# Optimization experiments

Hardware: AMD Instinct MI355X
Metric: run time of the kernel (lower is better)

The kernel has to match this reference:

```python
import jax, jax.numpy as jnp
import numpy as np
from jax import lax

# mamba-130m-hf config
N_LAYERS = 24
D_MODEL = 768
D_INNER = 1536   # expand=2
D_STATE = 16
DT_RANK = 48     # ceil(768/16)
D_CONV = 4
VOCAB = 50280
ENC_DIM = 256
EPS = 1e-5
SEQ, BATCH = 512, 2  # input is (SEQ, BATCH, ENC_DIM); permute -> mamba batch=BATCH, seq=SEQ


def setup_inputs() -> dict:
    key = jax.random.key(0)
    ks = jax.random.split(key, 12)
    f = jnp.float32
    def rn(k, shape, scale=0.02):
        return (jax.random.normal(k, shape) * scale).astype(f)
    x = jax.random.normal(ks[0], (SEQ, BATCH, ENC_DIM), dtype=f)
    W_et = rn(ks[1], (D_MODEL, ENC_DIM))
    b_et = jnp.zeros((D_MODEL,), f)
    in_proj_w = rn(ks[2], (N_LAYERS, 2 * D_INNER, D_MODEL))
    conv_w = rn(ks[3], (N_LAYERS, D_INNER, D_CONV), 0.1)
    conv_b = jnp.zeros((N_LAYERS, D_INNER), f)
    x_proj_w = rn(ks[4], (N_LAYERS, DT_RANK + 2 * D_STATE, D_INNER))
    dt_proj_w = rn(ks[5], (N_LAYERS, D_INNER, DT_RANK), 0.1)
    # bias init so softplus(bias) lands in [1e-3, 1e-1] (standard mamba dt init)
    dt_init = jnp.exp(jax.random.uniform(ks[6], (N_LAYERS, D_INNER), minval=jnp.log(1e-3), maxval=jnp.log(1e-1)))
    dt_proj_b = jnp.log(jnp.expm1(dt_init)).astype(f)
    A_log = jnp.log(jnp.broadcast_to(jnp.arange(1, D_STATE + 1, dtype=f), (N_LAYERS, D_INNER, D_STATE))) * jnp.ones((1,), f)
    D = jnp.ones((N_LAYERS, D_INNER), f)
    out_proj_w = rn(ks[7], (N_LAYERS, D_MODEL, D_INNER))
    norm_w = jnp.ones((N_LAYERS, D_MODEL), f)
    final_norm_w = jnp.ones((D_MODEL,), f)
    embed = rn(ks[8], (VOCAB, D_MODEL))
    return {"x": x, "W_et": W_et, "b_et": b_et, "in_proj_w": in_proj_w, "conv_w": conv_w,
            "conv_b": conv_b, "x_proj_w": x_proj_w, "dt_proj_w": dt_proj_w, "dt_proj_b": dt_proj_b,
            "A_log": A_log, "D": D, "out_proj_w": out_proj_w, "norm_w": norm_w,
            "final_norm_w": final_norm_w, "embed": embed}


def rmsnorm(x, w):
    return x * lax.rsqrt(jnp.mean(x * x, axis=-1, keepdims=True) + EPS) * w


def mamba_layer(h, p):
    in_w, cw, cb, xw, dtw, dtb, Al, Dv, ow, nw = p
    hn = rmsnorm(h, nw)
    xz = hn @ in_w.T                       # (B,T,2*D_INNER)
    xi, z = jnp.split(xz, 2, axis=-1)
    # depthwise causal conv over time
    xc = lax.conv_general_dilated(xi.transpose(0, 2, 1), cw[:, None, :], (1,),
                                  [(D_CONV - 1, 0)], dimension_numbers=("NCH", "OIH", "NCH"),
                                  feature_group_count=D_INNER)
    xc = jax.nn.silu(xc + cb[None, :, None]).transpose(0, 2, 1)   # (B,T,D_INNER)
    proj = xc @ xw.T                                              # (B,T,DT_RANK+2*D_STATE)
    dt = jax.nn.softplus(proj[..., :DT_RANK] @ dtw.T + dtb)       # (B,T,D_INNER)
    Bm = proj[..., DT_RANK:DT_RANK + D_STATE]                     # (B,T,S)
    Cm = proj[..., DT_RANK + D_STATE:]                            # (B,T,S)
    A = -jnp.exp(Al)                                              # (D_INNER,S)
    dA = jnp.exp(dt[..., None] * A)                               # (B,T,D,S)
    dBx = dt[..., None] * Bm[:, :, None, :] * xc[..., None]       # (B,T,D,S)

    def step(hst, inp):
        a, bx, c = inp
        hst = a * hst + bx
        return hst, jnp.einsum("bds,bs->bd", hst, c)

    h0 = jnp.zeros(dA.shape[:1] + dA.shape[2:], dA.dtype)
    _, ys = lax.scan(step, h0, (dA.transpose(1, 0, 2, 3), dBx.transpose(1, 0, 2, 3), Cm.transpose(1, 0, 2)))
    y = ys.transpose(1, 0, 2) + Dv * xc
    y = y * jax.nn.silu(z)
    return h + y @ ow.T


def reference(x, W_et, b_et, in_proj_w, conv_w, conv_b, x_proj_w, dt_proj_w, dt_proj_b,
              A_log, D, out_proj_w, norm_w, final_norm_w, embed):
    h = (x @ W_et.T + b_et).transpose(1, 0, 2)   # permute(1,0,2): (B,T,D_MODEL)

    def body(hc, p):
        return mamba_layer(hc, p), None

    h, _ = lax.scan(body, h, (in_proj_w, conv_w, conv_b, x_proj_w, dt_proj_w,
                              dt_proj_b, A_log, D, out_proj_w, norm_w))
    h = rmsnorm(h, final_norm_w)
    return h @ embed.T                            # tied lm_head logits (B,T,VOCAB)
```

## Files before the change

### kernel.cpp

```cpp
#include <hip/hip_runtime.h>
#include <math.h>

#define N_LAYERS 24
#define D_MODEL 768
#define D_INNER 1536
#define D_STATE 16
#define DT_RANK 48
#define D_CONV 4
#define VOCAB 50280
#define ENC_DIM 256
#define SEQ 512
#define BATCH 2
#define NTOK (SEQ*BATCH)
#define XZ_DIM (2*D_INNER)
#define PROJ_DIM (DT_RANK + 2*D_STATE)
#define DTW_PAD 64
#define IN_SPLIT 2
#define XP_SPLIT 8
#define OP_SPLIT 4

typedef __attribute__((ext_vector_type(8))) short bf16x8;
typedef __attribute__((ext_vector_type(4))) float f32x4;

__device__ __forceinline__ float sigmoidf_(float x) { return 1.f / (1.f + __expf(-x)); }
__device__ __forceinline__ float softplusf_(float x) {
    return fmaxf(x, 0.f) + log1pf(__expf(-fabsf(x)));
}
__device__ __forceinline__ short f2bf(float f) {
    unsigned u = __float_as_uint(f);
    unsigned r = (u + 0x7FFFu + ((u >> 16) & 1u)) >> 16;
    return (short)r;
}
__device__ __forceinline__ float bf2f(short s) {
    return __uint_as_float(((unsigned)(unsigned short)s) << 16);
}
__device__ __forceinline__ void load_lds16(const void* g, void* l) {
    __builtin_amdgcn_global_load_lds((const __attribute__((address_space(1))) void*)g,
                                     (__attribute__((address_space(3))) void*)l, 16, 0, 0);
}

__global__ __launch_bounds__(256) void cvt_k(const float* __restrict__ s,
                                             short* __restrict__ d, int n) {
    int stride = gridDim.x * 256 * 4;
    for (int i = (blockIdx.x * 256 + threadIdx.x) * 4; i + 3 < n; i += stride) {
        float4 f = *(const float4*)(s + i);
        short4 o; o.x = f2bf(f.x); o.y = f2bf(f.y); o.z = f2bf(f.z); o.w = f2bf(f.w);
        *(short4*)(d + i) = o;
    }
}

__global__ __launch_bounds__(256) void pad_dtw_k(const float* __restrict__ src,
                                                 short* __restrict__ dst) {
    int i = blockIdx.x * 256 + threadIdx.x;
    if (i >= N_LAYERS * D_INNER * DTW_PAD) return;
    int k = i & (DTW_PAD - 1);
    int rest = i >> 6;
    dst[i] = (k < DT_RANK) ? f2bf(src[(size_t)rest * DT_RANK + k]) : (short)0;
}

__global__ __launch_bounds__(256) void transpose_x_k(const float* __restrict__ x,
                                                     float* __restrict__ xt) {
    int i = blockIdx.x * 256 + threadIdx.x;
    if (i >= SEQ * BATCH * ENC_DIM) return;
    int e = i % ENC_DIM;
    int b = (i / ENC_DIM) % BATCH;
    int l = i / (ENC_DIM * BATCH);
    xt[((size_t)(b * SEQ + l)) * ENC_DIM + e] = x[i];
}
__global__ __launch_bounds__(256) void transpose_x_bf_k(const float* __restrict__ x,
                                                        short* __restrict__ xt) {
    int i = blockIdx.x * 256 + threadIdx.x;
    if (i >= SEQ * BATCH * ENC_DIM) return;
    int e = i % ENC_DIM;
    int b = (i / ENC_DIM) % BATCH;
    int l = i / (ENC_DIM * BATCH);
    xt[((size_t)(b * SEQ + l)) * ENC_DIM + e] = f2bf(x[i]);
}

__device__ __forceinline__ float rms_scale(const float* r, int tid) {
    float s = 0.f;
    for (int i = tid; i < D_MODEL; i += 256) { float v = r[i]; s += v * v; }
    for (int o = 32; o > 0; o >>= 1) s += __shfl_down(s, o);
    __shared__ float wsum[4];
    if ((tid & 63) == 0) wsum[tid >> 6] = s;
    __syncthreads();
    float tot = wsum[0] + wsum[1] + wsum[2] + wsum[3];
    return rsqrtf(tot / (float)D_MODEL + 1e-5f);
}
__global__ __launch_bounds__(256) void rmsnorm_k(const float* __restrict__ in,
                                                 const float* __restrict__ w,
                                                 float* __restrict__ out) {
    int row = blockIdx.x;
    const float* r = in + (size_t)row * D_MODEL;
    float sc = rms_scale(r, threadIdx.x);
    for (int i = threadIdx.x; i < D_MODEL; i += 256)
        out[(size_t)row * D_MODEL + i] = r[i] * sc * w[i];
}
__global__ __launch_bounds__(256) void rmsnorm_bf_k(const float* __restrict__ in,
                                                    const float* __restrict__ w,
                                                    short* __restrict__ out) {
    int row = blockIdx.x;
    const float* r = in + (size_t)row * D_MODEL;
    float sc = rms_scale(r, threadIdx.x);
    for (int i = threadIdx.x; i < D_MODEL; i += 256)
        out[(size_t)row * D_MODEL + i] = f2bf(r[i] * sc * w[i]);
}

template<int MODE, int BM, int DEPTH>
__global__ __launch_bounds__(256)
void gemm_p2(const short* __restrict__ A, const short* __restrict__ B,
             const float* __restrict__ bias, float* __restrict__ C,
             short* __restrict__ Cb,
             int M, int N, int K, int ldaE, int ldbE, int ldc, int ldcb)
{
    constexpr int NBUF = DEPTH + 1;
    constexpr int MI = BM / 32;
    constexpr int AELEM = 4 * BM;
    constexpr int BELEM = 4 * 128;
    constexpr int LA = AELEM / 256;
    constexpr int LB = BELEM / 256;
    constexpr int L = LA + LB;
    __shared__ short lA[NBUF][AELEM * 8];
    __shared__ short lB[NBUF][BELEM * 8];

    const int nx = gridDim.x;
    int lin = blockIdx.y * nx + blockIdx.x;
    const int nwg = nx * gridDim.y;
    if ((nwg & 7) == 0) { const int cpx = nwg >> 3; lin = (lin & 7) * cpx + (lin >> 3); }
    const int bm = (lin % nx) * BM;
    const int bn = (lin / nx) * 128;
    const int koff = blockIdx.z * K;

    const int t = threadIdx.x;
    const int wave = t >> 6;
    const int wm = (wave >> 1) * (BM / 2), wn = (wave & 1) * 64;
    const int l15 = t & 15, l4 = (t & 63) >> 4;

    f32x4 acc[MI][4] = {};
    const int nkt = K / 32;

    auto stage = [&](int buf, int kt) {
        const int k0 = koff + kt * 32;
        #pragma unroll
        for (int u = 0; u < LA; ++u) {
            const int idx = t + u * 256;
            const int kg = idx / BM;
            const int row = idx % BM;
            load_lds16(A + (size_t)(bm + row) * ldaE + k0 + kg * 8,
                       &lA[buf][(wave * 64 + u * 256) * 8]);
        }
        #pragma unroll
        for (int u = 0; u < LB; ++u) {
            const int idx = t + u * 256;
            const int kg = idx >> 7;
            const int row = idx & 127;
            int brow = bn + row; if (brow >= N) brow = 0;
            load_lds16(B + (size_t)brow * ldbE + k0 + kg * 8,
                       &lB[buf][(wave * 64 + u * 256) * 8]);
        }
    };

    #pragma unroll
    for (int p = 0; p < DEPTH; ++p)
        if (p < nkt) stage(p, p);

    for (int kt = 0; kt < nkt; ++kt) {
        const int rem = nkt - 1 - kt;
        const int ahead = rem < (DEPTH - 1) ? rem : (DEPTH - 1);
        if (ahead == 2) {
            if constexpr (L == 3) asm volatile("s_waitcnt vmcnt(6)" ::: "memory");
            else                  asm volatile("s_waitcnt vmcnt(8)" ::: "memory");
        } else if (ahead == 1) {
            if constexpr (L == 3) asm volatile("s_waitcnt vmcnt(3)" ::: "memory");
            else                  asm volatile("s_waitcnt vmcnt(4)" ::: "memory");
        } else {
            asm volatile("s_waitcnt vmcnt(0)" ::: "memory");
        }
        __builtin_amdgcn_s_barrier();
        __builtin_amdgcn_sched_barrier(0);
        if (kt + DEPTH < nkt) stage((kt + DEPTH) % NBUF, kt + DEPTH);
        const int cbuf = kt % NBUF;
        const short* bA = lA[cbuf];
        const short* bB = lB[cbuf];
        bf16x8 af[MI], bfr[4];
        #pragma unroll
        for (int i = 0; i < MI; ++i)
            af[i] = *(const bf16x8*)&bA[(l4 * BM + wm + i * 16 + l15) * 8];
        #pragma unroll
        for (int j = 0; j < 4; ++j)
            bfr[j] = *(const bf16x8*)&bB[(l4 * 128 + wn + j * 16 + l15) * 8];
        #pragma unroll
        for (int i = 0; i < MI; ++i)
            #pragma unroll
            for (int j = 0; j < 4; ++j)
                acc[i][j] = __builtin_amdgcn_mfma_f32_16x16x32_bf16(
                    af[i], bfr[j], acc[i][j], 0, 0, 0);
    }

    float* Cp = (MODE == 5) ? C + (size_t)blockIdx.z * M * ldc : C;
    #pragma unroll
    for (int i = 0; i < MI; ++i) {
        #pragma unroll
        for (int r = 0; r < 4; ++r) {
            const int row = bm + wm + i * 16 + l4 * 4 + r;
            #pragma unroll
            for (int j = 0; j < 4; ++j) {
                const int col = bn + wn + j * 16 + l15;
                if (col < N) {
                    float v = acc[i][j][r];
                    if (MODE == 6) {
                        Cb[(size_t)row * ldcb + col] = f2bf(softplusf_(v + bias[col]));
                    } else {
                        if (MODE == 1) v += bias[col];
                        if (MODE == 2) v = softplusf_(v + bias[col]);
                        if (MODE == 3) v += C[(size_t)row * ldc + col];
                        Cp[(size_t)row * ldc + col] = v;
                        if (MODE == 4) Cb[(size_t)row * ldcb + col] = f2bf(v);
                    }
                }
            }
        }
    }
}

__global__ __launch_bounds__(256) void reduce_conv_k(const float* __restrict__ part,
                                                     const float* __restrict__ cw,
                                                     const float* __restrict__ cb,
                                                     short* __restrict__ xcb,
                                                     short* __restrict__ zb) {
    int idx = blockIdx.x * 256 + threadIdx.x;
    if (idx >= NTOK * XZ_DIM) return;
    int d3 = idx % XZ_DIM;
    int m  = idx / XZ_DIM;
    if (d3 < D_INNER) {
        int l = m % SEQ;
        float acc = cb[d3];
        #pragma unroll
        for (int j = 0; j < D_CONV; ++j) {
            int ll = l - (D_CONV - 1) + j;
            if (ll >= 0) {
                int mm = m - (D_CONV - 1) + j;
                float v = part[(size_t)mm * XZ_DIM + d3]
                        + part[(size_t)(NTOK + mm) * XZ_DIM + d3];
                acc = fmaf(cw[d3 * D_CONV + j], v, acc);
            }
        }
        float v = acc * sigmoidf_(acc);
        xcb[(size_t)m * D_INNER + d3] = f2bf(v);
    } else {
        int d = d3 - D_INNER;
        float z = part[(size_t)m * XZ_DIM + d3]
                + part[(size_t)(NTOK + m) * XZ_DIM + d3];
        zb[(size_t)m * D_INNER + d] = f2bf(z);
    }
}

__global__ __launch_bounds__(256) void reduce_xp_k(const float* __restrict__ part,
                                                   float* __restrict__ proj,
                                                   short* __restrict__ projb) {
    const int n4 = NTOK * PROJ_DIM / 4;
    int i = blockIdx.x * 256 + threadIdx.x;
    if (i >= n4) return;
    float4 s = ((const float4*)part)[i];
    #pragma unroll
    for (int p = 1; p < XP_SPLIT; ++p) {
        float4 v = ((const float4*)part)[i + p * n4];
        s.x += v.x; s.y += v.y; s.z += v.z; s.w += v.w;
    }
    ((float4*)proj)[i] = s;
    short4 o; o.x = f2bf(s.x); o.y = f2bf(s.y); o.z = f2bf(s.z); o.w = f2bf(s.w);
    ((short4*)projb)[i] = o;
}

__global__ __launch_bounds__(256) void reduce_rms_k(const float* __restrict__ part,
                                                    float* __restrict__ h,
                                                    const float* __restrict__ w,
                                                    short* __restrict__ hnb) {
    const int row = blockIdx.x;
    const int i = threadIdx.x;
    float4 s = make_float4(0.f, 0.f, 0.f, 0.f);
    if (i < 192) {
        s = ((const float4*)h)[row * 192 + i];
        #pragma unroll
        for (int p = 0; p < OP_SPLIT; ++p) {
            float4 v = ((const float4*)part)[((size_t)p * NTOK + row) * 192 + i];
            s.x += v.x; s.y += v.y; s.z += v.z; s.w += v.w;
        }
        ((float4*)h)[row * 192 + i] = s;
    }
    float ss = s.x * s.x + s.y * s.y + s.z * s.z + s.w * s.w;
    for (int o = 32; o > 0; o >>= 1) ss += __shfl_down(ss, o);
    __shared__ float wsum[4];
    if ((i & 63) == 0) wsum[i >> 6] = ss;
    __syncthreads();
    float tot = wsum[0] + wsum[1] + wsum[2] + wsum[3];
    float sc = rsqrtf(tot / (float)D_MODEL + 1e-5f);
    if (i < 192) {
        float4 w4 = ((const float4*)w)[i];
        short4 o4;
        o4.x = f2bf(s.x * sc * w4.x); o4.y = f2bf(s.y * sc * w4.y);
        o4.z = f2bf(s.z * sc * w4.z); o4.w = f2bf(s.w * sc * w4.w);
        ((short4*)hnb)[row * 192 + i] = o4;
    }
}

template<int MODE>
__global__ __launch_bounds__(256)
void gemm_bf16(const float* __restrict__ A, const float* __restrict__ B,
               const float* __restrict__ bias, float* __restrict__ C,
               int M, int N, int K, int lda, int ldb, int ldc)
{
    __shared__ short lA[4 * 128 * 8];
    __shared__ short lB[4 * 128 * 8];
    const int bm = blockIdx.x * 128;
    const int bn = blockIdx.y * 128;
    const int t = threadIdx.x;
    const int wave = t >> 6, lane = t & 63;
    const int wm = (wave >> 1) * 64, wn = (wave & 1) * 64;
    const int l15 = lane & 15, l4 = lane >> 4;
    const int row2 = t >> 1;
    const int khalf = (t & 1) * 16;
    const int kgbase = khalf >> 3;
    f32x4 acc[4][4] = {};
    const int nkt = (K + 31) / 32;
    for (int kt = 0; kt < nkt; ++kt) {
        const int k0 = kt * 32 + khalf;
        {
            short v[16];
            const float* src = A + (size_t)(bm + row2) * lda + k0;
            if (k0 + 16 <= K) {
                #pragma unroll
                for (int j = 0; j < 16; j += 4) {
                    float4 f = *(const float4*)(src + j);
                    v[j+0]=f2bf(f.x); v[j+1]=f2bf(f.y); v[j+2]=f2bf(f.z); v[j+3]=f2bf(f.w);
                }
            } else {
                #pragma unroll
                for (int j = 0; j < 16; ++j)
                    v[j] = (k0 + j < K) ? f2bf(src[j]) : (short)0;
            }
            short* dst = &lA[(kgbase * 128 + row2) * 8];
            *(bf16x8*)dst = *(const bf16x8*)&v[0];
            *(bf16x8*)(dst + 128 * 8) = *(const bf16x8*)&v[8];
        }
        {
            short v[16];
            const int nrow = bn + row2;
            if (nrow < N) {
                const float* src = B + (size_t)nrow * ldb + k0;
                if (k0 + 16 <= K) {
                    #pragma unroll
                    for (int j = 0; j < 16; j += 4) {
                        float4 f = *(const float4*)(src + j);
                        v[j+0]=f2bf(f.x); v[j+1]=f2bf(f.y); v[j+2]=f2bf(f.z); v[j+3]=f2bf(f.w);
                    }
                } else {
                    #pragma unroll
                    for (int j = 0; j < 16; ++j)
                        v[j] = (k0 + j < K) ? f2bf(src[j]) : (short)0;
                }
            } else {
                #pragma unroll
                for (int j = 0; j < 16; ++j) v[j] = 0;
            }
            short* dst = &lB[(kgbase * 128 + row2) * 8];
            *(bf16x8*)dst = *(const bf16x8*)&v[0];
            *(bf16x8*)(dst + 128 * 8) = *(const bf16x8*)&v[8];
        }
        __syncthreads();
        bf16x8 af[4], bfr[4];
        #pragma unroll
        for (int i = 0; i < 4; ++i)
            af[i] = *(const bf16x8*)&lA[(l4 * 128 + wm + i * 16 + l15) * 8];
        #pragma unroll
        for (int j = 0; j < 4; ++j)
            bfr[j] = *(const bf16x8*)&lB[(l4 * 128 + wn + j * 16 + l15) * 8];
        #pragma unroll
        for (int i = 0; i < 4; ++i)
            #pragma unroll
            for (int j = 0; j < 4; ++j)
                acc[i][j] = __builtin_amdgcn_mfma_f32_16x16x32_bf16(
                    af[i], bfr[j], acc[i][j], 0, 0, 0);
        __syncthreads();
    }
    #pragma unroll
    for (int i = 0; i < 4; ++i) {
        #pragma unroll
        for (int r = 0; r < 4; ++r) {
            const int row = bm + wm + i * 16 + l4 * 4 + r;
            #pragma unroll
            for (int j = 0; j < 4; ++j) {
                const int col = bn + wn + j * 16 + l15;
                if (col < N) {
                    float v = acc[i][j][r];
                    if (MODE == 1) v += bias[col];
                    if (MODE == 2) v = softplusf_(v + bias[col]);
                    if (MODE == 3) v += C[(size_t)row * ldc + col];
                    C[(size_t)row * ldc + col] = v;
                }
            }
        }
    }
}

template<int DUAL>
__global__ __launch_bounds__(256) void conv_silu_k(const float* __restrict__ xz,
                                                   const float* __restrict__ cw,
                                                   const float* __restrict__ cb,
                                                   float* __restrict__ xc,
                                                   short* __restrict__ xcb) {
    int idx = blockIdx.x * 256 + threadIdx.x;
    if (idx >= NTOK * D_INNER) return;
    int d = idx % D_INNER;
    int m = idx / D_INNER;
    int l = m % SEQ;
    float acc = cb[d];
    #pragma unroll
    for (int j = 0; j < D_CONV; ++j) {
        int ll = l - (D_CONV - 1) + j;
        if (ll >= 0)
            acc = fmaf(cw[d * D_CONV + j],
                       xz[(size_t)(m - (D_CONV - 1) + j) * XZ_DIM + d], acc);
    }
    float v = acc * sigmoidf_(acc);
    xc[(size_t)m * D_INNER + d] = v;
    if (DUAL) xcb[(size_t)m * D_INNER + d] = f2bf(v);
}

#define SCAN_DW 16
#define SCAN_NC 32
#define SCAN_CL (SEQ / SCAN_NC)
template<int BF>
__global__ __launch_bounds__(512) void scan3_k(const float* __restrict__ proj,
                                               const void* __restrict__ dtp,
                                               const void* __restrict__ xcp,
                                               const void* __restrict__ zp,
                                               int zld,
                                               const float* __restrict__ A_log,
                                               const float* __restrict__ Dvec,
                                               void* __restrict__ yout) {
    __shared__ float lp[D_STATE][SCAN_NC][SCAN_DW];
    __shared__ float ls[D_STATE][SCAN_NC][SCAN_DW];
    const int nblk_d = D_INNER / SCAN_DW;
    const int b  = blockIdx.x / nblk_d;
    const int d0 = (blockIdx.x % nblk_d) * SCAN_DW;
    const int t  = threadIdx.x;
    const int dl = t & (SCAN_DW - 1);
    const int c  = t >> 4;
    const int d  = d0 + dl;

    float A[D_STATE];
    #pragma unroll
    for (int s = 0; s < D_STATE; s += 4) {
        float4 a4 = *(const float4*)&A_log[(size_t)d * D_STATE + s];
        A[s+0] = -__expf(a4.x); A[s+1] = -__expf(a4.y);
        A[s+2] = -__expf(a4.z); A[s+3] = -__expf(a4.w);
    }
    const int m0 = b * SEQ + c * SCAN_CL;

    float P[D_STATE], S[D_STATE];
    #pragma unroll
    for (int s = 0; s < D_STATE; ++s) { P[s] = 1.f; S[s] = 0.f; }
    for (int i = 0; i < SCAN_CL; ++i) {
        const int m = m0 + i;
        float dtv, xcv;
        if (BF) {
            dtv = bf2f(((const short*)dtp)[(size_t)m * D_INNER + d]);
            xcv = bf2f(((const short*)xcp)[(size_t)m * D_INNER + d]);
        } else {
            dtv = ((const float*)dtp)[(size_t)m * D_INNER + d];
            xcv = ((const float*)xcp)[(size_t)m * D_INNER + d];
        }
        float dx = dtv * xcv;
        const float* pB = proj + (size_t)m * PROJ_DIM + DT_RANK;
        float Bv[D_STATE];
        #pragma unroll
        for (int s = 0; s < D_STATE; s += 4)
            *(float4*)&Bv[s] = *(const float4*)(pB + s);
        #pragma unroll
        for (int s = 0; s < D_STATE; ++s) {
            float da = __expf(dtv * A[s]);
            S[s] = fmaf(da, S[s], dx * Bv[s]);
            P[s] *= da;
        }
    }
    #pragma unroll
    for (int s = 0; s < D_STATE; ++s) { lp[s][c][dl] = P[s]; ls[s][c][dl] = S[s]; }
    __syncthreads();

    float st[D_STATE];
    #pragma unroll
    for (int s = 0; s < D_STATE; ++s) st[s] = 0.f;
    for (int j = 0; j < c; ++j) {
        #pragma unroll
        for (int s = 0; s < D_STATE; ++s)
            st[s] = fmaf(lp[s][j][dl], st[s], ls[s][j][dl]);
    }

    const float Dvv = Dvec[d];
    for (int i = 0; i < SCAN_CL; ++i) {
        const int m = m0 + i;
        float dtv, xcv, zv;
        if (BF) {
            dtv = bf2f(((const short*)dtp)[(size_t)m * D_INNER + d]);
            xcv = bf2f(((const short*)xcp)[(size_t)m * D_INNER + d]);
            zv  = bf2f(((const short*)zp)[(size_t)m * zld + d]);
        } else {
            dtv = ((const float*)dtp)[(size_t)m * D_INNER + d];
            xcv = ((const float*)xcp)[(size_t)m * D_INNER + d];
            zv  = ((const float*)zp)[(size_t)m * zld + d];
        }
        float dx = dtv * xcv;
        const float* pB = proj + (size_t)m * PROJ_DIM + DT_RANK;
        float Bv[D_STATE], Cv[D_STATE];
        #pragma unroll
        for (int s = 0; s < D_STATE; s += 4) {
            *(float4*)&Bv[s] = *(const float4*)(pB + s);
            *(float4*)&Cv[s] = *(const float4*)(pB + D_STATE + s);
        }
        float acc = Dvv * xcv;
        #pragma unroll
        for (int s = 0; s < D_STATE; ++s) {
            float da = __expf(dtv * A[s]);
            st[s] = fmaf(da, st[s], dx * Bv[s]);
            acc = fmaf(st[s], Cv[s], acc);
        }
        float yv = acc * (zv * sigmoidf_(zv));
        if (BF) ((short*)yout)[(size_t)m * D_INNER + d] = f2bf(yv);
        else    ((float*)yout)[(size_t)m * D_INNER + d] = yv;
    }
}

extern "C" void kernel_launch(void* const* d_in, const int* in_sizes, int n_in,
                              void* d_out, int out_size, void* d_ws, size_t ws_size,
                              hipStream_t stream) {
    const float* x           = (const float*)d_in[0];
    const float* W_et        = (const float*)d_in[1];
    const float* b_et        = (const float*)d_in[2];
    const float* in_proj_w   = (const float*)d_in[3];
    const float* conv_w      = (const float*)d_in[4];
    const float* conv_b      = (const float*)d_in[5];
    const float* x_proj_w    = (const float*)d_in[6];
    const float* dt_proj_w   = (const float*)d_in[7];
    const float* dt_proj_b   = (const float*)d_in[8];
    const float* A_log       = (const float*)d_in[9];
    const float* Dv          = (const float*)d_in[10];
    const float* out_proj_w  = (const float*)d_in[11];
    const float* norm_w      = (const float*)d_in[12];
    const float* final_norm_w= (const float*)d_in[13];
    const float* embed       = (const float*)d_in[14];
    float* out = (float*)d_out;
    float* ws  = (float*)d_ws;

    float* h       = ws;
    float* proj    = h + (size_t)NTOK * D_MODEL;
    float* scratch = proj + (size_t)NTOK * PROJ_DIM;
    short* xt_bf   = (short*)(scratch + (size_t)IN_SPLIT * NTOK * XZ_DIM);
    short* hn_bf   = xt_bf   + (size_t)NTOK * ENC_DIM;
    short* xc_bf   = hn_bf   + (size_t)NTOK * D_MODEL;
    short* z_bf    = xc_bf   + (size_t)NTOK * D_INNER;
    short* dt_bf   = z_bf    + (size_t)NTOK * D_INNER;
    short* proj_bf = dt_bf   + (size_t)NTOK * D_INNER;
    short* yb_bf   = proj_bf + (size_t)NTOK * PROJ_DIM;
    short* wet_bf  = yb_bf   + (size_t)NTOK * D_INNER;
    short* inw_bf  = wet_bf  + (size_t)D_MODEL * ENC_DIM;
    short* xw_bf   = inw_bf  + (size_t)N_LAYERS * XZ_DIM * D_MODEL;
    short* dtw_bf  = xw_bf   + (size_t)N_LAYERS * PROJ_DIM * D_INNER;
    short* ow_bf   = dtw_bf  + (size_t)N_LAYERS * D_INNER * DTW_PAD;
    short* emb_bf  = ow_bf   + (size_t)N_LAYERS * D_MODEL * D_INNER;
    short* end_bf  = emb_bf  + (size_t)VOCAB * D_MODEL;
    size_t needA = (size_t)((char*)end_bf - (char*)d_ws);
    bool tierA = ws_size >= needA;

    dim3 blk(256);
    const int scan_blocks = BATCH * (D_INNER / SCAN_DW);

    if (tierA) {
        auto cvt = [&](const float* s, short* d, size_t n) {
            int nb = (int)((n / 4 + 255) / 256); if (nb > 2048) nb = 2048;
            cvt_k<<<nb, blk, 0, stream>>>(s, d, (int)n);
        };
        cvt(W_et, wet_bf, (size_t)D_MODEL * ENC_DIM);
        cvt(in_proj_w, inw_bf, (size_t)N_LAYERS * XZ_DIM * D_MODEL);
        cvt(x_proj_w, xw_bf, (size_t)N_LAYERS * PROJ_DIM * D_INNER);
        cvt(out_proj_w, ow_bf, (size_t)N_LAYERS * D_MODEL * D_INNER);
        cvt(embed, emb_bf, (size_t)VOCAB * D_MODEL);
        pad_dtw_k<<<(N_LAYERS * D_INNER * DTW_PAD + 255) / 256, blk, 0, stream>>>(
            dt_proj_w, dtw_bf);

        transpose_x_bf_k<<<(SEQ * BATCH * ENC_DIM + 255) / 256, blk, 0, stream>>>(x, xt_bf);
        gemm_p2<1, 64, 2><<<dim3(NTOK / 64, D_MODEL / 128), blk, 0, stream>>>(
            xt_bf, wet_bf, b_et, h, nullptr,
            NTOK, D_MODEL, ENC_DIM, ENC_DIM, ENC_DIM, D_MODEL, 0);
        rmsnorm_bf_k<<<NTOK, blk, 0, stream>>>(h, norm_w, hn_bf);

        for (int L = 0; L < N_LAYERS; ++L) {
            const short* in_w = inw_bf + (size_t)L * XZ_DIM * D_MODEL;
            const float* cw   = conv_w + (size_t)L * D_INNER * D_CONV;
            const float* cb   = conv_b + (size_t)L * D_INNER;
            const short* xw   = xw_bf  + (size_t)L * PROJ_DIM * D_INNER;
            const short* dtw  = dtw_bf + (size_t)L * D_INNER * DTW_PAD;
            const float* dtbp = dt_proj_b + (size_t)L * D_INNER;
            const float* Al   = A_log  + (size_t)L * D_INNER * D_STATE;
            const float* Dl   = Dv     + (size_t)L * D_INNER;
            const short* ow   = ow_bf  + (size_t)L * D_MODEL * D_INNER;
            const float* nw_next = (L == N_LAYERS - 1) ? final_norm_w
                                 : norm_w + (size_t)(L + 1) * D_MODEL;

            gemm_p2<5, 64, 3><<<dim3(NTOK / 64, XZ_DIM / 128, IN_SPLIT), blk, 0, stream>>>(
                hn_bf, in_w, nullptr, scratch, nullptr,
                NTOK, XZ_DIM, D_MODEL / IN_SPLIT, D_MODEL, D_MODEL, XZ_DIM, 0);
            reduce_conv_k<<<(NTOK * XZ_DIM + 255) / 256, blk, 0, stream>>>(
                scratch, cw, cb, xc_bf, z_bf);
            gemm_p2<5, 64, 3><<<dim3(NTOK / 64, 1, XP_SPLIT), blk, 0, stream>>>(
                xc_bf, xw, nullptr, scratch, nullptr,
                NTOK, PROJ_DIM, D_INNER / XP_SPLIT, D_INNER, D_INNER, PROJ_DIM, 0);
            reduce_xp_k<<<(NTOK * PROJ_DIM / 4 + 255) / 256, blk, 0, stream>>>(
                scratch, proj, proj_bf);
            gemm_p2<6, 64, 2><<<dim3(NTOK / 64, D_INNER / 128), blk, 0, stream>>>(
                proj_bf, dtw, dtbp, h , dt_bf,
                NTOK, D_INNER, DTW_PAD, PROJ_DIM, DTW_PAD, D_INNER, D_INNER);
            scan3_k<1><<<scan_blocks, dim3(512), 0, stream>>>(
                proj, dt_bf, xc_bf, z_bf, D_INNER, Al, Dl, yb_bf);
            gemm_p2<5, 64, 3><<<dim3(NTOK / 64, D_MODEL / 128, OP_SPLIT), blk, 0, stream>>>(
                yb_bf, ow, nullptr, scratch, nullptr,
                NTOK, D_MODEL, D_INNER / OP_SPLIT, D_INNER, D_INNER, D_MODEL, 0);
            reduce_rms_k<<<NTOK, blk, 0, stream>>>(scratch, h, nw_next, hn_bf);
        }

        gemm_p2<0, 128, 2><<<dim3(NTOK / 128, (VOCAB + 127) / 128), blk, 0, stream>>>(
            hn_bf, emb_bf, nullptr, out, nullptr,
            NTOK, VOCAB, D_MODEL, D_MODEL, D_MODEL, VOCAB, 0);
    } else {
        float* hB   = ws;
        float* hnB  = hB   + (size_t)NTOK * D_MODEL;
        float* xzB  = hnB  + (size_t)NTOK * D_MODEL;
        float* xcB  = xzB  + (size_t)NTOK * XZ_DIM;
        float* projB= xcB  + (size_t)NTOK * D_INNER;
        float* dtB  = projB+ (size_t)NTOK * PROJ_DIM;
        float* ybB  = dtB  + (size_t)NTOK * D_INNER;

        transpose_x_k<<<(SEQ * BATCH * ENC_DIM + 255) / 256, blk, 0, stream>>>(x, ybB);
        gemm_bf16<1><<<dim3(NTOK / 128, D_MODEL / 128), blk, 0, stream>>>(
            ybB, W_et, b_et, hB, NTOK, D_MODEL, ENC_DIM, ENC_DIM, ENC_DIM, D_MODEL);
        for (int L = 0; L < N_LAYERS; ++L) {
            const float* in_w = in_proj_w  + (size_t)L * XZ_DIM * D_MODEL;
            const float* cw   = conv_w     + (size_t)L * D_INNER * D_CONV;
            const float* cb   = conv_b     + (size_t)L * D_INNER;
            const float* xw   = x_proj_w   + (size_t)L * PROJ_DIM * D_INNER;
            const float* dtw  = dt_proj_w  + (size_t)L * D_INNER * DT_RANK;
            const float* dtbp = dt_proj_b  + (size_t)L * D_INNER;
            const float* Al   = A_log      + (size_t)L * D_INNER * D_STATE;
            const float* Dl   = Dv         + (size_t)L * D_INNER;
            const float* ow   = out_proj_w + (size_t)L * D_MODEL * D_INNER;
            const float* nw   = norm_w     + (size_t)L * D_MODEL;
            rmsnorm_k<<<NTOK, blk, 0, stream>>>(hB, nw, hnB);
            gemm_bf16<0><<<dim3(NTOK / 128, XZ_DIM / 128), blk, 0, stream>>>(
                hnB, in_w, nullptr, xzB, NTOK, XZ_DIM, D_MODEL, D_MODEL, D_MODEL, XZ_DIM);
            conv_silu_k<0><<<(NTOK * D_INNER + 255) / 256, blk, 0, stream>>>(
                xzB, cw, cb, xcB, nullptr);
            gemm_bf16<0><<<dim3(NTOK / 128, 1), blk, 0, stream>>>(
                xcB, xw, nullptr, projB, NTOK, PROJ_DIM, D_INNER, D_INNER, D_INNER, PROJ_DIM);
            gemm_bf16<2><<<dim3(NTOK / 128, D_INNER / 128), blk, 0, stream>>>(
                projB, dtw, dtbp, dtB, NTOK, D_INNER, DT_RANK, PROJ_DIM, DT_RANK, D_INNER);
            scan3_k<0><<<scan_blocks, dim3(512), 0, stream>>>(
                projB, dtB, xcB, xzB + D_INNER, XZ_DIM, Al, Dl, ybB);
            gemm_bf16<3><<<dim3(NTOK / 128, D_MODEL / 128), blk, 0, stream>>>(
                ybB, ow, nullptr, hB, NTOK, D_MODEL, D_INNER, D_INNER, D_INNER, D_MODEL);
        }
        rmsnorm_k<<<NTOK, blk, 0, stream>>>(hB, final_norm_w, hnB);
        gemm_bf16<0><<<dim3(NTOK / 128, (VOCAB + 127) / 128), blk, 0, stream>>>(
            hnB, embed, nullptr, out, NTOK, VOCAB, D_MODEL, D_MODEL, D_MODEL, VOCAB);
    }
}
```

Measured before the change: 3.011 ms.

## Fuse dt projection into scan kernel, generalize XCD remap, enlarge lm_head tile

Removes the separate dt_proj GEMM and its bf16 dt buffer: each scan thread now computes the 48-wide dt dot product in registers from fp32 proj and applies softplus itself, in both scan passes. The aim is to save one launch plus the round trip of dt through memory each layer, at the cost of recomputing the dot twice per token. The XCD-aware block remap now also handles workgroup counts that are not a multiple of 8, and the vmcnt waits are templated. The final vocab GEMM uses BM=256 tiles, which raises LDS use and register pressure.

```diff
diff --git a/kernel.cpp b/kernel.cpp
--- a/kernel.cpp
+++ b/kernel.cpp
@@ -38,6 +38,15 @@
     __builtin_amdgcn_global_load_lds((const __attribute__((address_space(1))) void*)g,
                                      (__attribute__((address_space(3))) void*)l, 16, 0, 0);
 }
+template<int V> __device__ __forceinline__ void vwait() {
+    if constexpr (V == 0)       asm volatile("s_waitcnt vmcnt(0)" ::: "memory");
+    else if constexpr (V == 3)  asm volatile("s_waitcnt vmcnt(3)" ::: "memory");
+    else if constexpr (V == 4)  asm volatile("s_waitcnt vmcnt(4)" ::: "memory");
+    else if constexpr (V == 6)  asm volatile("s_waitcnt vmcnt(6)" ::: "memory");
+    else if constexpr (V == 8)  asm volatile("s_waitcnt vmcnt(8)" ::: "memory");
+    else if constexpr (V == 12) asm volatile("s_waitcnt vmcnt(12)" ::: "memory");
+    else                        asm volatile("s_waitcnt vmcnt(0)" ::: "memory");
+}
 
 __global__ __launch_bounds__(256) void cvt_k(const float* __restrict__ s,
                                              short* __restrict__ d, int n) {
@@ -126,7 +135,11 @@
     const int nx = gridDim.x;
     int lin = blockIdx.y * nx + blockIdx.x;
     const int nwg = nx * gridDim.y;
-    if ((nwg & 7) == 0) { const int cpx = nwg >> 3; lin = (lin & 7) * cpx + (lin >> 3); }
+    {
+        const int q = nwg >> 3, r = nwg & 7;
+        const int xcd = lin & 7, win = lin >> 3;
+        lin = (xcd < r ? xcd * (q + 1) : r * (q + 1) + (xcd - r) * q) + win;
+    }
     const int bm = (lin % nx) * BM;
     const int bn = (lin / nx) * 128;
     const int koff = blockIdx.z * K;
@@ -167,15 +180,9 @@
     for (int kt = 0; kt < nkt; ++kt) {
         const int rem = nkt - 1 - kt;
         const int ahead = rem < (DEPTH - 1) ? rem : (DEPTH - 1);
-        if (ahead == 2) {
-            if constexpr (L == 3) asm volatile("s_waitcnt vmcnt(6)" ::: "memory");
-            else                  asm volatile("s_waitcnt vmcnt(8)" ::: "memory");
-        } else if (ahead == 1) {
-            if constexpr (L == 3) asm volatile("s_waitcnt vmcnt(3)" ::: "memory");
-            else                  asm volatile("s_waitcnt vmcnt(4)" ::: "memory");
-        } else {
-            asm volatile("s_waitcnt vmcnt(0)" ::: "memory");
-        }
+        if (ahead == 2)      vwait<2 * L>();
+        else if (ahead == 1) vwait<L>();
+        else                 vwait<0>();
         __builtin_amdgcn_s_barrier();
         __builtin_amdgcn_sched_barrier(0);
         if (kt + DEPTH < nkt) stage((kt + DEPTH) % NBUF, kt + DEPTH);
@@ -256,8 +263,7 @@
 }
 
 __global__ __launch_bounds__(256) void reduce_xp_k(const float* __restrict__ part,
-                                                   float* __restrict__ proj,
-                                                   short* __restrict__ projb) {
+                                                   float* __restrict__ proj) {
     const int n4 = NTOK * PROJ_DIM / 4;
     int i = blockIdx.x * 256 + threadIdx.x;
     if (i >= n4) return;
@@ -268,8 +274,6 @@
         s.x += v.x; s.y += v.y; s.z += v.z; s.w += v.w;
     }
     ((float4*)proj)[i] = s;
-    short4 o; o.x = f2bf(s.x); o.y = f2bf(s.y); o.z = f2bf(s.z); o.w = f2bf(s.w);
-    ((short4*)projb)[i] = o;
 }
 
 __global__ __launch_bounds__(256) void reduce_rms_k(const float* __restrict__ part,
@@ -430,6 +434,117 @@
 #define SCAN_DW 16
 #define SCAN_NC 32
 #define SCAN_CL (SEQ / SCAN_NC)
+__device__ __forceinline__ float dt_dot(const float* pr, const bf16x8* w6,
+                                        float bias) {
+    float dot = bias;
+    #pragma unroll
+    for (int kk = 0; kk < 6; ++kk) {
+        float4 p0 = *(const float4*)(pr + kk * 8);
+        float4 p1 = *(const float4*)(pr + kk * 8 + 4);
+        dot = fmaf(p0.x, bf2f(w6[kk][0]), dot);
+        dot = fmaf(p0.y, bf2f(w6[kk][1]), dot);
+        dot = fmaf(p0.z, bf2f(w6[kk][2]), dot);
+        dot = fmaf(p0.w, bf2f(w6[kk][3]), dot);
+        dot = fmaf(p1.x, bf2f(w6[kk][4]), dot);
+        dot = fmaf(p1.y, bf2f(w6[kk][5]), dot);
+        dot = fmaf(p1.z, bf2f(w6[kk][6]), dot);
+        dot = fmaf(p1.w, bf2f(w6[kk][7]), dot);
+    }
+    return softplusf_(dot);
+}
+__global__ __launch_bounds__(512) void scan4_k(const float* __restrict__ proj,
+                                               const short* __restrict__ dtw,
+                                               const float* __restrict__ dtb,
+                                               const short* __restrict__ xcp,
+                                               const short* __restrict__ zp,
+                                               const float* __restrict__ A_log,
+                                               const float* __restrict__ Dvec,
+                                               short* __restrict__ yout) {
+    __shared__ float lp[D_STATE][SCAN_NC][SCAN_DW];
+    __shared__ float ls[D_STATE][SCAN_NC][SCAN_DW];
+    const int nblk_d = D_INNER / SCAN_DW;
+    const int b  = blockIdx.x / nblk_d;
+    const int d0 = (blockIdx.x % nblk_d) * SCAN_DW;
+    const int t  = threadIdx.x;
+    const int dl = t & (SCAN_DW - 1);
+    const int c  = t >> 4;
+    const int d  = d0 + dl;
+
+    float A[D_STATE];
+    #pragma unroll
+    for (int s = 0; s < D_STATE; s += 4) {
+        float4 a4 = *(const float4*)&A_log[(size_t)d * D_STATE + s];
+        A[s+0] = -__expf(a4.x); A[s+1] = -__expf(a4.y);
+        A[s+2] = -__expf(a4.z); A[s+3] = -__expf(a4.w);
+    }
+    bf16x8 w6[6];
+    {
+        const short* wr = dtw + (size_t)d * DTW_PAD;
+        #pragma unroll
+        for (int kk = 0; kk < 6; ++kk) w6[kk] = *(const bf16x8*)(wr + kk * 8);
+    }
+    const float dtbias = dtb[d];
+    const int m0 = b * SEQ + c * SCAN_CL;
+
+    float P[D_STATE], S[D_STATE];
+    #pragma unroll
+    for (int s = 0; s < D_STATE; ++s) { P[s] = 1.f; S[s] = 0.f; }
+    for (int i = 0; i < SCAN_CL; ++i) {
+        const int m = m0 + i;
+        const float* pr = proj + (size_t)m * PROJ_DIM;
+        float dtv = dt_dot(pr, w6, dtbias);
+        float xcv = bf2f(xcp[(size_t)m * D_INNER + d]);
+        float dx = dtv * xcv;
+        float Bv[D_STATE];
+        #pragma unroll
+        for (int s = 0; s < D_STATE; s += 4)
+            *(float4*)&Bv[s] = *(const float4*)(pr + DT_RANK + s);
+        #pragma unroll
+        for (int s = 0; s < D_STATE; ++s) {
+            float da = __expf(dtv * A[s]);
+            S[s] = fmaf(da, S[s], dx * Bv[s]);
+            P[s] *= da;
+        }
+    }
+    #pragma unroll
+    for (int s = 0; s < D_STATE; ++s) { lp[s][c][dl] = P[s]; ls[s][c][dl] = S[s]; }
+    __syncthreads();
+
+    float st[D_STATE];
+    #pragma unroll
+    for (int s = 0; s < D_STATE; ++s) st[s] = 0.f;
+    for (int j = 0; j < c; ++j) {
+        #pragma unroll
+        for (int s = 0; s < D_STATE; ++s)
+            st[s] = fmaf(lp[s][j][dl], st[s], ls[s][j][dl]);
+    }
+
+    const float Dvv = Dvec[d];
+    for (int i = 0; i < SCAN_CL; ++i) {
+        const int m = m0 + i;
+        const float* pr = proj + (size_t)m * PROJ_DIM;
+        float dtv = dt_dot(pr, w6, dtbias);
+        float xcv = bf2f(xcp[(size_t)m * D_INNER + d]);
+        float zv  = bf2f(zp[(size_t)m * D_INNER + d]);
+        float dx = dtv * xcv;
+        float Bv[D_STATE], Cv[D_STATE];
+        #pragma unroll
+        for (int s = 0; s < D_STATE; s += 4) {
+            *(float4*)&Bv[s] = *(const float4*)(pr + DT_RANK + s);
+            *(float4*)&Cv[s] = *(const float4*)(pr + DT_RANK + D_STATE + s);
+        }
+        float acc = Dvv * xcv;
+        #pragma unroll
+        for (int s = 0; s < D_STATE; ++s) {
+            float da = __expf(dtv * A[s]);
+            st[s] = fmaf(da, st[s], dx * Bv[s]);
+            acc = fmaf(st[s], Cv[s], acc);
+        }
+        float yv = acc * (zv * sigmoidf_(zv));
+        yout[(size_t)m * D_INNER + d] = f2bf(yv);
+    }
+}
+
 template<int BF>
 __global__ __launch_bounds__(512) void scan3_k(const float* __restrict__ proj,
                                                const void* __restrict__ dtp,
@@ -463,14 +578,8 @@
     for (int s = 0; s < D_STATE; ++s) { P[s] = 1.f; S[s] = 0.f; }
     for (int i = 0; i < SCAN_CL; ++i) {
         const int m = m0 + i;
-        float dtv, xcv;
-        if (BF) {
-            dtv = bf2f(((const short*)dtp)[(size_t)m * D_INNER + d]);
-            xcv = bf2f(((const short*)xcp)[(size_t)m * D_INNER + d]);
-        } else {
-            dtv = ((const float*)dtp)[(size_t)m * D_INNER + d];
-            xcv = ((const float*)xcp)[(size_t)m * D_INNER + d];
-        }
+        float dtv = ((const float*)dtp)[(size_t)m * D_INNER + d];
+        float xcv = ((const float*)xcp)[(size_t)m * D_INNER + d];
         float dx = dtv * xcv;
         const float* pB = proj + (size_t)m * PROJ_DIM + DT_RANK;
         float Bv[D_STATE];
@@ -500,16 +609,9 @@
     const float Dvv = Dvec[d];
     for (int i = 0; i < SCAN_CL; ++i) {
         const int m = m0 + i;
-        float dtv, xcv, zv;
-        if (BF) {
-            dtv = bf2f(((const short*)dtp)[(size_t)m * D_INNER + d]);
-            xcv = bf2f(((const short*)xcp)[(size_t)m * D_INNER + d]);
-            zv  = bf2f(((const short*)zp)[(size_t)m * zld + d]);
-        } else {
-            dtv = ((const float*)dtp)[(size_t)m * D_INNER + d];
-            xcv = ((const float*)xcp)[(size_t)m * D_INNER + d];
-            zv  = ((const float*)zp)[(size_t)m * zld + d];
-        }
+        float dtv = ((const float*)dtp)[(size_t)m * D_INNER + d];
+        float xcv = ((const float*)xcp)[(size_t)m * D_INNER + d];
+        float zv  = ((const float*)zp)[(size_t)m * zld + d];
         float dx = dtv * xcv;
         const float* pB = proj + (size_t)m * PROJ_DIM + DT_RANK;
         float Bv[D_STATE], Cv[D_STATE];
@@ -526,8 +628,7 @@
             acc = fmaf(st[s], Cv[s], acc);
         }
         float yv = acc * (zv * sigmoidf_(zv));
-        if (BF) ((short*)yout)[(size_t)m * D_INNER + d] = f2bf(yv);
-        else    ((float*)yout)[(size_t)m * D_INNER + d] = yv;
+        ((float*)yout)[(size_t)m * D_INNER + d] = yv;
     }
 }
 
@@ -559,9 +660,7 @@
     short* hn_bf   = xt_bf   + (size_t)NTOK * ENC_DIM;
     short* xc_bf   = hn_bf   + (size_t)NTOK * D_MODEL;
     short* z_bf    = xc_bf   + (size_t)NTOK * D_INNER;
-    short* dt_bf   = z_bf    + (size_t)NTOK * D_INNER;
-    short* proj_bf = dt_bf   + (size_t)NTOK * D_INNER;
-    short* yb_bf   = proj_bf + (size_t)NTOK * PROJ_DIM;
+    short* yb_bf   = z_bf    + (size_t)NTOK * D_INNER;
     short* wet_bf  = yb_bf   + (size_t)NTOK * D_INNER;
     short* inw_bf  = wet_bf  + (size_t)D_MODEL * ENC_DIM;
     short* xw_bf   = inw_bf  + (size_t)N_LAYERS * XZ_DIM * D_MODEL;
@@ -616,19 +715,16 @@
                 xc_bf, xw, nullptr, scratch, nullptr,
                 NTOK, PROJ_DIM, D_INNER / XP_SPLIT, D_INNER, D_INNER, PROJ_DIM, 0);
             reduce_xp_k<<<(NTOK * PROJ_DIM / 4 + 255) / 256, blk, 0, stream>>>(
-                scratch, proj, proj_bf);
-            gemm_p2<6, 64, 2><<<dim3(NTOK / 64, D_INNER / 128), blk, 0, stream>>>(
-                proj_bf, dtw, dtbp, h , dt_bf,
-                NTOK, D_INNER, DTW_PAD, PROJ_DIM, DTW_PAD, D_INNER, D_INNER);
-            scan3_k<1><<<scan_blocks, dim3(512), 0, stream>>>(
-                proj, dt_bf, xc_bf, z_bf, D_INNER, Al, Dl, yb_bf);
+                scratch, proj);
+            scan4_k<<<scan_blocks, dim3(512), 0, stream>>>(
+                proj, dtw, dtbp, xc_bf, z_bf, Al, Dl, yb_bf);
             gemm_p2<5, 64, 3><<<dim3(NTOK / 64, D_MODEL / 128, OP_SPLIT), blk, 0, stream>>>(
                 yb_bf, ow, nullptr, scratch, nullptr,
                 NTOK, D_MODEL, D_INNER / OP_SPLIT, D_INNER, D_INNER, D_MODEL, 0);
             reduce_rms_k<<<NTOK, blk, 0, stream>>>(scratch, h, nw_next, hn_bf);
         }
 
-        gemm_p2<0, 128, 2><<<dim3(NTOK / 128, (VOCAB + 127) / 128), blk, 0, stream>>>(
+        gemm_p2<0, 256, 2><<<dim3(NTOK / 256, (VOCAB + 127) / 128), blk, 0, stream>>>(
             hn_bf, emb_bf, nullptr, out, nullptr,
             NTOK, VOCAB, D_MODEL, D_MODEL, D_MODEL, VOCAB, 0);
     } else {
```

Result: slower. 3.345 ms (+11.1%).
